# Kernel optimization log

Measured on AMD Instinct MI355X. Metric: run time of the kernel, lower is better.

## Reference

```python
import jax, jax.numpy as jnp
import numpy as np

DIM = 384
HEADS = 6
DIM_HEAD = 64
INNER = HEADS * DIM_HEAD  # 384


def setup_inputs() -> dict:
    key = jax.random.key(0)
    ks = jax.random.split(key, 6)
    s = 0.02
    return {
        "x_q": jax.random.normal(ks[0], (8, 4096, DIM), dtype=jnp.float32),
        "x_kv": jax.random.normal(ks[1], (8, 4096, DIM), dtype=jnp.float32),
        "Wq": jax.random.normal(ks[2], (DIM, INNER), dtype=jnp.float32) * s,
        "Wkv": jax.random.normal(ks[3], (DIM, 2 * INNER), dtype=jnp.float32) * s,
        "Wout": jax.random.normal(ks[4], (INNER, DIM), dtype=jnp.float32) * s,
        "bout": jax.random.normal(ks[5], (DIM,), dtype=jnp.float32) * s,
    }


def _split_heads(t, b, n):
    # [b, n, h*d] -> [b, h, n, d]
    return t.reshape(b, n, HEADS, DIM_HEAD).transpose(0, 2, 1, 3)


def reference(x_q, x_kv, Wq, Wkv, Wout, bout):
    b, nq, _ = x_q.shape
    nkv = x_kv.shape[1]
    q = x_q @ Wq                      # [b, nq, inner]
    kv_proj = x_kv @ Wkv              # [b, nkv, 2*inner]
    k, v = jnp.split(kv_proj, 2, axis=-1)
    q = _split_heads(q, b, nq)        # [b, h, nq, d]
    k = _split_heads(k, b, nkv)       # [b, h, nkv, d]
    v = _split_heads(v, b, nkv)       # [b, h, nkv, d]
    q = jax.nn.elu(q) + 1.0
    k = jax.nn.elu(k) + 1.0
    kv = jnp.einsum('bhnd,bhnm->bhdm', k, v)             # [b, h, d, d]
    z = 1.0 / (jnp.einsum('bhnd,bhd->bhn', q, k.sum(axis=2)) + 1e-6)
    out = jnp.einsum('bhnd,bhdm->bhnm', q, kv) * z[..., None]  # [b, h, nq, d]
    out = out.transpose(0, 2, 1, 3).reshape(b, nq, INNER)
    return out @ Wout + bout
```

## Files before the change

### kernel.cpp

```cpp
#include <hip/hip_runtime.h>
#include <math.h>

#define BATCH 8
#define SEQ 4096
#define DIMSZ 384
#define HEADS 6
#define DH 64
#define MTOT (BATCH * SEQ)
#define KD 384

typedef short short8 __attribute__((ext_vector_type(8)));
typedef float floatx4 __attribute__((ext_vector_type(4)));
typedef unsigned short ushort8v __attribute__((ext_vector_type(8)));
typedef unsigned int uint2v __attribute__((ext_vector_type(2)));
typedef unsigned int uint4v __attribute__((ext_vector_type(4)));

__device__ __forceinline__ float elu1(float x) { return x > 0.f ? x + 1.f : __expf(x); }

__device__ __forceinline__ unsigned short f2b(float f) {
    unsigned int u = __float_as_uint(f);
    u = (u + 0x7fffu + ((u >> 16) & 1u)) >> 16;
    return (unsigned short)u;
}
__device__ __forceinline__ unsigned int f2b2(float lo, float hi) {
    unsigned int r;
    asm("v_cvt_pk_bf16_f32 %0, %1, %2" : "=v"(r) : "v"(lo), "v"(hi));
    return r;
}

__device__ __forceinline__ void gl16(const void* g, void* l) {
    __builtin_amdgcn_global_load_lds((const __attribute__((address_space(1))) unsigned int*)g,
                                     (__attribute__((address_space(3))) unsigned int*)l, 16, 0, 0);
}

#define SB0() __builtin_amdgcn_sched_barrier(0)
#define BAR_SOFT()                     \
    do {                               \
        SB0();                         \
        __builtin_amdgcn_s_barrier();  \
        SB0();                         \
    } while (0)
#define BAR_STAGE()                                                 \
    do {                                                            \
        asm volatile("s_waitcnt vmcnt(0) lgkmcnt(0)" ::: "memory"); \
        __builtin_amdgcn_s_barrier();                               \
        SB0();                                                      \
    } while (0)

__global__ __launch_bounds__(256) void conv_wt3(const float* __restrict__ Wq,
                                                const float* __restrict__ Wkv,
                                                const float* __restrict__ Wout,
                                                unsigned short* __restrict__ WqT,
                                                unsigned short* __restrict__ WkvT,
                                                unsigned short* __restrict__ WoutT) {
    __shared__ float tile[32][33];
    int bx = blockIdx.x;
    const float* W;
    unsigned short* WT;
    int N;
    if (bx < 12) { W = Wq; WT = WqT; N = DIMSZ; }
    else if (bx < 36) { W = Wkv; WT = WkvT; N = 2 * DIMSZ; bx -= 12; }
    else { W = Wout; WT = WoutT; N = DIMSZ; bx -= 36; }
    const int n0 = bx * 32, k0 = blockIdx.y * 32;
    const int tx = threadIdx.x & 31, ty = threadIdx.x >> 5;
#pragma unroll
    for (int i = 0; i < 32; i += 8) tile[ty + i][tx] = W[(size_t)(k0 + ty + i) * N + n0 + tx];
    __syncthreads();
#pragma unroll
    for (int i = 0; i < 32; i += 8)
        WT[(size_t)(n0 + ty + i) * KD + k0 + tx] = f2b(tile[tx][ty + i]);
}

__global__ __launch_bounds__(256, 3) void gemm_kv(const float* __restrict__ A,
                                                  const unsigned short* __restrict__ WkvT,
                                                  float* __restrict__ pkv,
                                                  float* __restrict__ pks) {
    __shared__ __align__(16) unsigned short buf[24576];
    __shared__ float ksLDS[128];
    unsigned short* As = buf;
    unsigned short* Bs0 = buf + 8192;
    unsigned short* Bs1 = buf + 16384;
    const int tid = threadIdx.x;
    const int lane = tid & 63, wave = tid >> 6;
    const int l15 = lane & 15, qd = lane >> 4;
    const int fid = blockIdx.x;
    const int xcd = fid & 7;
    const int s = fid >> 3;
    const int h = s % HEADS;
    const int rtl = s / HEADS;
    const int row0 = (xcd * 32 + rtl) * 128;
    const int pidx = (xcd * HEADS + h) * 32 + rtl;
    const int wm = (wave & 1) * 64, wn = (wave >> 1) * 64;

    const float* Ab = A + (size_t)row0 * KD;
    const unsigned short* Bb = WkvT + (size_t)(h * DH) * KD;
    const int srow = tid >> 3;
    const int scol = (((tid & 7) ^ (srow & 7)) * 8);

    floatx4 zero = {0.f, 0.f, 0.f, 0.f};
    floatx4 acc[4][4];
#pragma unroll
    for (int i = 0; i < 4; ++i)
#pragma unroll
        for (int j = 0; j < 4; ++j) acc[i][j] = zero;

    const int sw = l15 & 7;
    float4 g0[4], g1[4];
#pragma unroll
    for (int i = 0; i < 4; ++i)
        gl16(Bb + (size_t)(i * 32 + srow + (i >= 2 ? 320 : 0)) * KD + scol,
             Bs0 + i * 2048 + wave * 512);
#pragma unroll
    for (int i = 0; i < 4; ++i) {
        const float* src = Ab + (size_t)(i * 32 + srow) * KD + scol;
        g0[i] = *(const float4*)src;
        g1[i] = *(const float4*)(src + 4);
    }
#pragma unroll
    for (int i = 0; i < 4; ++i) {
        uint4v u;
        u[0] = f2b2(g0[i].x, g0[i].y);
        u[1] = f2b2(g0[i].z, g0[i].w);
        u[2] = f2b2(g1[i].x, g1[i].y);
        u[3] = f2b2(g1[i].z, g1[i].w);
        *(uint4v*)&As[i * 2048 + tid * 8] = u;
    }
    BAR_STAGE();

#pragma unroll
    for (int t = 0; t < 6; ++t) {
        unsigned short* Bc = (t & 1) ? Bs1 : Bs0;
        if (t < 5) {
            unsigned short* Bn = (t & 1) ? Bs0 : Bs1;
            const int kn = t * 64 + 64;
#pragma unroll
            for (int i = 0; i < 4; ++i)
                gl16(Bb + (size_t)(i * 32 + srow + (i >= 2 ? 320 : 0)) * KD + kn + scol,
                     Bn + i * 2048 + wave * 512);
#pragma unroll
            for (int i = 0; i < 4; ++i) {
                const float* src = Ab + (size_t)(i * 32 + srow) * KD + kn + scol;
                g0[i] = *(const float4*)src;
                g1[i] = *(const float4*)(src + 4);
            }
            SB0();
        }
#pragma unroll
        for (int tt = 0; tt < 2; ++tt) {
            const int chnk = ((tt * 4 + qd) ^ sw) * 8;
            short8 af[4], bfr[4];
#pragma unroll
            for (int mi = 0; mi < 4; ++mi)
                af[mi] = *(const short8*)&As[(wm + mi * 16 + l15) * 64 + chnk];
#pragma unroll
            for (int ni = 0; ni < 4; ++ni)
                bfr[ni] = *(const short8*)&Bc[(wn + ni * 16 + l15) * 64 + chnk];
#pragma unroll
            for (int mi = 0; mi < 4; ++mi)
#pragma unroll
                for (int ni = 0; ni < 4; ++ni)
                    acc[mi][ni] = __builtin_amdgcn_mfma_f32_16x16x32_bf16(af[mi], bfr[ni],
                                                                          acc[mi][ni], 0, 0, 0);
        }
        if (t < 5) {
            BAR_SOFT();
#pragma unroll
            for (int i = 0; i < 4; ++i) {
                uint4v u;
                u[0] = f2b2(g0[i].x, g0[i].y);
                u[1] = f2b2(g0[i].z, g0[i].w);
                u[2] = f2b2(g1[i].x, g1[i].y);
                u[3] = f2b2(g1[i].z, g1[i].w);
                *(uint4v*)&As[i * 2048 + tid * 8] = u;
            }
            BAR_STAGE();
        }
    }

    __syncthreads();
    const bool kw = (wn == 0);
    float ksp[4] = {};
#pragma unroll
    for (int mi = 0; mi < 4; ++mi)
#pragma unroll
        for (int ni = 0; ni < 4; ++ni) {
            const int rb = wm + mi * 16 + qd * 4;
            const int cl = wn + ni * 16 + l15;
            float v0 = acc[mi][ni][0], v1 = acc[mi][ni][1];
            float v2 = acc[mi][ni][2], v3 = acc[mi][ni][3];
            if (kw) {
                v0 = elu1(v0); v1 = elu1(v1); v2 = elu1(v2); v3 = elu1(v3);
                ksp[ni] += (v0 + v1) + (v2 + v3);
            }
            uint2v o;
            o[0] = f2b2(v0, v1);
            o[1] = f2b2(v2, v3);
            *(uint2v*)&buf[cl * 136 + rb] = o;
        }
    if (kw) {
#pragma unroll
        for (int ni = 0; ni < 4; ++ni) {
            float v = ksp[ni];
            v += __shfl_xor(v, 16);
            v += __shfl_xor(v, 32);
            if (lane < 16) ksLDS[wave * 64 + ni * 16 + lane] = v;
        }
    }
    __syncthreads();
    floatx4 kva[4];
#pragma unroll
    for (int j = 0; j < 4; ++j) kva[j] = zero;
#pragma unroll
    for (int nk = 0; nk < 4; ++nk) {
        short8 afk = *(const short8*)&buf[(wave * 16 + l15) * 136 + nk * 32 + qd * 8];
#pragma unroll
        for (int nj = 0; nj < 4; ++nj) {
            short8 bfv = *(const short8*)&buf[(64 + nj * 16 + l15) * 136 + nk * 32 + qd * 8];
            kva[nj] = __builtin_amdgcn_mfma_f32_16x16x32_bf16(afk, bfv, kva[nj], 0, 0, 0);
        }
    }
    float* P = pkv + (size_t)pidx * 4096;
#pragma unroll
    for (int nj = 0; nj < 4; ++nj)
#pragma unroll
        for (int r = 0; r < 4; ++r)
            P[(wave * 16 + qd * 4 + r) * 64 + nj * 16 + l15] = kva[nj][r];
    if (tid < 64) pks[pidx * 64 + tid] = ksLDS[tid] + ksLDS[64 + tid];
}

__global__ __launch_bounds__(256) void kv_reduce(const float* __restrict__ pkv,
                                                 const float* __restrict__ pks,
                                                 unsigned short* __restrict__ kv_bf,
                                                 float* __restrict__ ksum_g) {
    const int bh = blockIdx.x >> 2, dc = blockIdx.x & 3;
    const int tid = threadIdx.x;
    unsigned short* kb = kv_bf + (size_t)bh * 4096;
    const int i0 = dc * 1024 + tid * 4;
    float4 sum = {0.f, 0.f, 0.f, 0.f};
#pragma unroll
    for (int c = 0; c < 32; ++c) {
        float4 p = *(const float4*)&pkv[(size_t)(bh * 32 + c) * 4096 + i0];
        sum.x += p.x; sum.y += p.y; sum.z += p.z; sum.w += p.w;
    }
    const int d = i0 >> 6, m = i0 & 63;
    kb[(m + 0) * 64 + d] = f2b(sum.x);
    kb[(m + 1) * 64 + d] = f2b(sum.y);
    kb[(m + 2) * 64 + d] = f2b(sum.z);
    kb[(m + 3) * 64 + d] = f2b(sum.w);
    if (dc == 0 && tid < 64) {
        float s = 0.f;
#pragma unroll
        for (int c = 0; c < 32; ++c) s += pks[(bh * 32 + c) * 64 + tid];
        ksum_g[bh * 64 + tid] = s;
    }
}

__global__ __launch_bounds__(256, 3) void gemm_q_attn(const float* __restrict__ A,
                                                      const unsigned short* __restrict__ WqT,
                                                      const unsigned short* __restrict__ kv_bf,
                                                      const float* __restrict__ ksum_g,
                                                      unsigned short* __restrict__ attn) {
    __shared__ __align__(16) unsigned short buf[24576];
    __shared__ float ksh[128];
    __shared__ float zsh[256];
    unsigned short* As = buf;
    unsigned short* Bs0 = buf + 8192;
    unsigned short* Bs1 = buf + 16384;
    const int tid = threadIdx.x;
    const int lane = tid & 63, wave = tid >> 6;
    const int l15 = lane & 15, qd = lane >> 4;
    const int fid = blockIdx.x;
    const int xcd = fid & 7;
    const int s = fid >> 3;
    const int ct = s % 3;
    const int rtl = s / 3;
    const int row0 = (xcd * 32 + rtl) * 128;
    const int col0 = ct * 128;
    const int bh0 = xcd * HEADS + ct * 2;
    const int wd = (wave & 1) * 64, wn2 = (wave >> 1) * 64;

    if (tid < 128) ksh[tid] = ksum_g[bh0 * 64 + tid];

    const float* Ab = A + (size_t)row0 * KD;
    const unsigned short* Bb = WqT + (size_t)col0 * KD;
    const int srow = tid >> 3;
    const int scol = (((tid & 7) ^ (srow & 7)) * 8);

    floatx4 zero = {0.f, 0.f, 0.f, 0.f};
    floatx4 acc[4][4];
#pragma unroll
    for (int i = 0; i < 4; ++i)
#pragma unroll
        for (int j = 0; j < 4; ++j) acc[i][j] = zero;

    const int sw = l15 & 7;
    float4 g0[4], g1[4];
#pragma unroll
    for (int i = 0; i < 4; ++i)
        gl16(Bb + (size_t)(i * 32 + srow) * KD + scol, Bs0 + i * 2048 + wave * 512);
#pragma unroll
    for (int i = 0; i < 4; ++i) {
        const float* src = Ab + (size_t)(i * 32 + srow) * KD + scol;
        g0[i] = *(const float4*)src;
        g1[i] = *(const float4*)(src + 4);
    }
#pragma unroll
    for (int i = 0; i < 4; ++i) {
        uint4v u;
        u[0] = f2b2(g0[i].x, g0[i].y);
        u[1] = f2b2(g0[i].z, g0[i].w);
        u[2] = f2b2(g1[i].x, g1[i].y);
        u[3] = f2b2(g1[i].z, g1[i].w);
        *(uint4v*)&As[i * 2048 + tid * 8] = u;
    }
    BAR_STAGE();

#pragma unroll
    for (int t = 0; t < 6; ++t) {
        unsigned short* Bc = (t & 1) ? Bs1 : Bs0;
        if (t < 5) {
            unsigned short* Bn = (t & 1) ? Bs0 : Bs1;
            const int kn = t * 64 + 64;
#pragma unroll
            for (int i = 0; i < 4; ++i)
                gl16(Bb + (size_t)(i * 32 + srow) * KD + kn + scol, Bn + i * 2048 + wave * 512);
#pragma unroll
            for (int i = 0; i < 4; ++i) {
                const float* src = Ab + (size_t)(i * 32 + srow) * KD + kn + scol;
                g0[i] = *(const float4*)src;
                g1[i] = *(const float4*)(src + 4);
            }
            SB0();
        }
#pragma unroll
        for (int tt = 0; tt < 2; ++tt) {
            const int chnk = ((tt * 4 + qd) ^ sw) * 8;
            short8 wf[4], xf[4];
#pragma unroll
            for (int di = 0; di < 4; ++di)
                wf[di] = *(const short8*)&Bc[(wd + di * 16 + l15) * 64 + chnk];
#pragma unroll
            for (int nj = 0; nj < 4; ++nj)
                xf[nj] = *(const short8*)&As[(wn2 + nj * 16 + l15) * 64 + chnk];
#pragma unroll
            for (int di = 0; di < 4; ++di)
#pragma unroll
                for (int nj = 0; nj < 4; ++nj)
                    acc[di][nj] = __builtin_amdgcn_mfma_f32_16x16x32_bf16(wf[di], xf[nj],
                                                                          acc[di][nj], 0, 0, 0);
        }
        if (t < 5) {
            BAR_SOFT();
#pragma unroll
            for (int i = 0; i < 4; ++i) {
                uint4v u;
                u[0] = f2b2(g0[i].x, g0[i].y);
                u[1] = f2b2(g0[i].z, g0[i].w);
                u[2] = f2b2(g1[i].x, g1[i].y);
                u[3] = f2b2(g1[i].z, g1[i].w);
                *(uint4v*)&As[i * 2048 + tid * 8] = u;
            }
            BAR_STAGE();
        }
    }

    float zp[4] = {};
#pragma unroll
    for (int di = 0; di < 4; ++di)
#pragma unroll
        for (int r = 0; r < 4; ++r) {
            const float ks = ksh[wd + di * 16 + qd * 4 + r];
#pragma unroll
            for (int nj = 0; nj < 4; ++nj) {
                const float q = elu1(acc[di][nj][r]);
                acc[di][nj][r] = q;
                zp[nj] += q * ks;
            }
        }
#pragma unroll
    for (int nj = 0; nj < 4; ++nj) {
        float v = zp[nj];
        v += __shfl_xor(v, 16);
        v += __shfl_xor(v, 32);
        zp[nj] = 1.f / (v + 1e-6f);
    }
    __syncthreads();
    if (lane < 16) {
#pragma unroll
        for (int nj = 0; nj < 4; ++nj) zsh[(wave & 1) * 128 + wn2 + nj * 16 + lane] = zp[nj];
    }
#pragma unroll
    for (int di = 0; di < 4; ++di)
#pragma unroll
        for (int nj = 0; nj < 4; ++nj) {
            const int rb = wd + di * 16 + qd * 4;
            const int cl = wn2 + nj * 16 + l15;
            uint2v o;
            o[0] = f2b2(acc[di][nj][0], acc[di][nj][1]);
            o[1] = f2b2(acc[di][nj][2], acc[di][nj][3]);
            *(uint2v*)&buf[cl * 136 + rb] = o;
        }
    __syncthreads();
    const int hh = wave & 1;
    const unsigned short* kvB = kv_bf + (size_t)(bh0 + hh) * 4096;
    floatx4 acc2[4][4];
#pragma unroll
    for (int i = 0; i < 4; ++i)
#pragma unroll
        for (int j = 0; j < 4; ++j) acc2[i][j] = zero;
#pragma unroll
    for (int t = 0; t < 2; ++t) {
        short8 bf2[4];
#pragma unroll
        for (int bj = 0; bj < 4; ++bj)
            bf2[bj] = *(const short8*)&kvB[(bj * 16 + l15) * 64 + t * 32 + qd * 8];
#pragma unroll
        for (int ai = 0; ai < 4; ++ai) {
            short8 af =
                *(const short8*)&buf[(wn2 + ai * 16 + l15) * 136 + hh * 64 + t * 32 + qd * 8];
#pragma unroll
            for (int bj = 0; bj < 4; ++bj)
                acc2[ai][bj] =
                    __builtin_amdgcn_mfma_f32_16x16x32_bf16(af, bf2[bj], acc2[ai][bj], 0, 0, 0);
        }
    }
#pragma unroll
    for (int ai = 0; ai < 4; ++ai)
#pragma unroll
        for (int bj = 0; bj < 4; ++bj) {
            const int colg = col0 + hh * 64 + bj * 16 + l15;
#pragma unroll
            for (int r = 0; r < 4; ++r) {
                const int nl = wn2 + ai * 16 + qd * 4 + r;
                const float v = acc2[ai][bj][r] * zsh[hh * 128 + nl];
                attn[(size_t)(row0 + nl) * KD + colg] = f2b(v);
            }
        }
}

__global__ __launch_bounds__(256, 3) void gemm_out(const unsigned short* __restrict__ A,
                                                   const unsigned short* __restrict__ BT,
                                                   float* __restrict__ C,
                                                   const float* __restrict__ bias) {
    __shared__ __align__(16) unsigned short buf[24576];
    unsigned short* As = buf;
    unsigned short* Bs0 = buf + 8192;
    unsigned short* Bs1 = buf + 16384;
    const int tid = threadIdx.x;
    const int lane = tid & 63, wave = tid >> 6;
    const int l15 = lane & 15, qd = lane >> 4;
    const int fid = blockIdx.x;
    const int xcd = fid & 7;
    const int s = fid >> 3;
    const int row0 = (xcd * 32 + s / 3) * 128;
    const int col0 = (s % 3) * 128;
    const int wm = (wave & 1) * 64, wn = (wave >> 1) * 64;

    const unsigned short* Ab = A + (size_t)row0 * KD;
    const unsigned short* Bb = BT + (size_t)col0 * KD;
    const int srow = tid >> 3;
    const int scol = (((tid & 7) ^ (srow & 7)) * 8);

    floatx4 zero = {0.f, 0.f, 0.f, 0.f};
    floatx4 acc[4][4];
#pragma unroll
    for (int i = 0; i < 4; ++i)
#pragma unroll
        for (int j = 0; j < 4; ++j) acc[i][j] = zero;

    const int sw = l15 & 7;
    ushort8v ga[4];
#pragma unroll
    for (int i = 0; i < 4; ++i)
        gl16(Bb + (size_t)(i * 32 + srow) * KD + scol, Bs0 + i * 2048 + wave * 512);
#pragma unroll
    for (int i = 0; i < 4; ++i)
        ga[i] = *(const ushort8v*)(Ab + (size_t)(i * 32 + srow) * KD + scol);
#pragma unroll
    for (int i = 0; i < 4; ++i) *(ushort8v*)&As[i * 2048 + tid * 8] = ga[i];
    BAR_STAGE();

#pragma unroll
    for (int t = 0; t < 6; ++t) {
        unsigned short* Bc = (t & 1) ? Bs1 : Bs0;
        if (t < 5) {
            unsigned short* Bn = (t & 1) ? Bs0 : Bs1;
            const int kn = t * 64 + 64;
#pragma unroll
            for (int i = 0; i < 4; ++i)
                gl16(Bb + (size_t)(i * 32 + srow) * KD + kn + scol, Bn + i * 2048 + wave * 512);
#pragma unroll
            for (int i = 0; i < 4; ++i)
                ga[i] = *(const ushort8v*)(Ab + (size_t)(i * 32 + srow) * KD + kn + scol);
            SB0();
        }
#pragma unroll
        for (int tt = 0; tt < 2; ++tt) {
            const int chnk = ((tt * 4 + qd) ^ sw) * 8;
            short8 af[4], bfr[4];
#pragma unroll
            for (int mi = 0; mi < 4; ++mi)
                af[mi] = *(const short8*)&As[(wm + mi * 16 + l15) * 64 + chnk];
#pragma unroll
            for (int ni = 0; ni < 4; ++ni)
                bfr[ni] = *(const short8*)&Bc[(wn + ni * 16 + l15) * 64 + chnk];
#pragma unroll
            for (int mi = 0; mi < 4; ++mi)
#pragma unroll
                for (int ni = 0; ni < 4; ++ni)
                    acc[mi][ni] = __builtin_amdgcn_mfma_f32_16x16x32_bf16(af[mi], bfr[ni],
                                                                          acc[mi][ni], 0, 0, 0);
        }
        if (t < 5) {
            BAR_SOFT();
#pragma unroll
            for (int i = 0; i < 4; ++i) *(ushort8v*)&As[i * 2048 + tid * 8] = ga[i];
            BAR_STAGE();
        }
    }
#pragma unroll
    for (int mi = 0; mi < 4; ++mi)
#pragma unroll
        for (int ni = 0; ni < 4; ++ni) {
            const int rbase = row0 + wm + mi * 16 + qd * 4;
            const int col = col0 + wn + ni * 16 + l15;
            const float bsv = bias[col];
#pragma unroll
            for (int r = 0; r < 4; ++r)
                __builtin_nontemporal_store(acc[mi][ni][r] + bsv,
                                            &C[(size_t)(rbase + r) * DIMSZ + col]);
        }
}

extern "C" void kernel_launch(void* const* d_in, const int* in_sizes, int n_in,
                              void* d_out, int out_size, void* d_ws, size_t ws_size,
                              hipStream_t stream) {
    const float* x_q = (const float*)d_in[0];
    const float* x_kv = (const float*)d_in[1];
    const float* Wq = (const float*)d_in[2];
    const float* Wkv = (const float*)d_in[3];
    const float* Wout = (const float*)d_in[4];
    const float* bout = (const float*)d_in[5];
    float* out = (float*)d_out;

    char* ws = (char*)d_ws;
    float* pkv = (float*)(ws + 0);
    unsigned short* attn_bf = (unsigned short*)(ws + 0);
    unsigned short* WqT = (unsigned short*)(ws + 25165824);
    unsigned short* WkvT = (unsigned short*)(ws + 25460736);
    unsigned short* WoutT = (unsigned short*)(ws + 26050560);
    float* ksum = (float*)(ws + 26345472);
    float* pks = (float*)(ws + 26357760);
    unsigned short* kv_bf = (unsigned short*)(ws + 26750976);

    dim3 blk(256);
    conv_wt3<<<dim3(48, 12), blk, 0, stream>>>(Wq, Wkv, Wout, WqT, WkvT, WoutT);
    gemm_kv<<<dim3(1536), blk, 0, stream>>>(x_kv, WkvT, pkv, pks);
    kv_reduce<<<dim3(192), blk, 0, stream>>>(pkv, pks, kv_bf, ksum);
    gemm_q_attn<<<dim3(768), blk, 0, stream>>>(x_q, WqT, kv_bf, ksum, attn_bf);
    gemm_out<<<dim3(768), blk, 0, stream>>>(attn_bf, WoutT, out, bout);
}
```

Before: 216.2 us.

## Double-buffer A tiles and stage B through registers, dropping one barrier per step

```diff
diff --git a/kernel.cpp b/kernel.cpp
--- a/kernel.cpp
+++ b/kernel.cpp
@@ -28,23 +28,12 @@
     return r;
 }
 
-__device__ __forceinline__ void gl16(const void* g, void* l) {
-    __builtin_amdgcn_global_load_lds((const __attribute__((address_space(1))) unsigned int*)g,
-                                     (__attribute__((address_space(3))) unsigned int*)l, 16, 0, 0);
-}
-
 #define SB0() __builtin_amdgcn_sched_barrier(0)
-#define BAR_SOFT()                     \
-    do {                               \
-        SB0();                         \
-        __builtin_amdgcn_s_barrier();  \
-        SB0();                         \
-    } while (0)
-#define BAR_STAGE()                                                 \
-    do {                                                            \
-        asm volatile("s_waitcnt vmcnt(0) lgkmcnt(0)" ::: "memory"); \
-        __builtin_amdgcn_s_barrier();                               \
-        SB0();                                                      \
+#define BAR_LGKM()                                        \
+    do {                                                  \
+        asm volatile("s_waitcnt lgkmcnt(0)" ::: "memory");\
+        __builtin_amdgcn_s_barrier();                     \
+        SB0();                                            \
     } while (0)
 
 __global__ __launch_bounds__(256) void conv_wt3(const float* __restrict__ Wq,
@@ -71,15 +60,16 @@
         WT[(size_t)(n0 + ty + i) * KD + k0 + tx] = f2b(tile[tx][ty + i]);
 }
 
-__global__ __launch_bounds__(256, 3) void gemm_kv(const float* __restrict__ A,
+__global__ __launch_bounds__(256, 2) void gemm_kv(const float* __restrict__ A,
                                                   const unsigned short* __restrict__ WkvT,
                                                   float* __restrict__ pkv,
                                                   float* __restrict__ pks) {
-    __shared__ __align__(16) unsigned short buf[24576];
+    __shared__ __align__(16) unsigned short buf[32768];
     __shared__ float ksLDS[128];
-    unsigned short* As = buf;
-    unsigned short* Bs0 = buf + 8192;
-    unsigned short* Bs1 = buf + 16384;
+    unsigned short* As0 = buf;
+    unsigned short* As1 = buf + 8192;
+    unsigned short* Bs0 = buf + 16384;
+    unsigned short* Bs1 = buf + 24576;
     const int tid = threadIdx.x;
     const int lane = tid & 63, wave = tid >> 6;
     const int l15 = lane & 15, qd = lane >> 4;
@@ -106,15 +96,13 @@
 
     const int sw = l15 & 7;
     float4 g0[4], g1[4];
-#pragma unroll
-    for (int i = 0; i < 4; ++i)
-        gl16(Bb + (size_t)(i * 32 + srow + (i >= 2 ? 320 : 0)) * KD + scol,
-             Bs0 + i * 2048 + wave * 512);
+    ushort8v gb[4];
 #pragma unroll
     for (int i = 0; i < 4; ++i) {
         const float* src = Ab + (size_t)(i * 32 + srow) * KD + scol;
         g0[i] = *(const float4*)src;
         g1[i] = *(const float4*)(src + 4);
+        gb[i] = *(const ushort8v*)(Bb + (size_t)(i * 32 + srow + (i >= 2 ? 320 : 0)) * KD + scol);
     }
 #pragma unroll
     for (int i = 0; i < 4; ++i) {
@@ -123,25 +111,27 @@
         u[1] = f2b2(g0[i].z, g0[i].w);
         u[2] = f2b2(g1[i].x, g1[i].y);
         u[3] = f2b2(g1[i].z, g1[i].w);
-        *(uint4v*)&As[i * 2048 + tid * 8] = u;
-    }
-    BAR_STAGE();
+        *(uint4v*)&As0[i * 2048 + tid * 8] = u;
+        *(ushort8v*)&Bs0[i * 2048 + tid * 8] = gb[i];
+    }
+    BAR_LGKM();
 
 #pragma unroll
     for (int t = 0; t < 6; ++t) {
+        unsigned short* Ac = (t & 1) ? As1 : As0;
         unsigned short* Bc = (t & 1) ? Bs1 : Bs0;
+        unsigned short* An = (t & 1) ? As0 : As1;
+        unsigned short* Bn = (t & 1) ? Bs0 : Bs1;
         if (t < 5) {
-            unsigned short* Bn = (t & 1) ? Bs0 : Bs1;
-            const int kn = t * 64 + 64;
-#pragma unroll
-            for (int i = 0; i < 4; ++i)
-                gl16(Bb + (size_t)(i * 32 + srow + (i >= 2 ? 320 : 0)) * KD + kn + scol,
-                     Bn + i * 2048 + wave * 512);
+            const int kn = (t + 1) * 64;
 #pragma unroll
             for (int i = 0; i < 4; ++i) {
                 const float* src = Ab + (size_t)(i * 32 + srow) * KD + kn + scol;
                 g0[i] = *(const float4*)src;
                 g1[i] = *(const float4*)(src + 4);
+                gb[i] = *(const ushort8v*)(Bb +
+                                           (size_t)(i * 32 + srow + (i >= 2 ? 320 : 0)) * KD +
+                                           kn + scol);
             }
             SB0();
         }
@@ -151,7 +141,7 @@
             short8 af[4], bfr[4];
 #pragma unroll
             for (int mi = 0; mi < 4; ++mi)
-                af[mi] = *(const short8*)&As[(wm + mi * 16 + l15) * 64 + chnk];
+                af[mi] = *(const short8*)&Ac[(wm + mi * 16 + l15) * 64 + chnk];
 #pragma unroll
             for (int ni = 0; ni < 4; ++ni)
                 bfr[ni] = *(const short8*)&Bc[(wn + ni * 16 + l15) * 64 + chnk];
@@ -163,7 +153,6 @@
                                                                           acc[mi][ni], 0, 0, 0);
         }
         if (t < 5) {
-            BAR_SOFT();
 #pragma unroll
             for (int i = 0; i < 4; ++i) {
                 uint4v u;
@@ -171,9 +160,10 @@
                 u[1] = f2b2(g0[i].z, g0[i].w);
                 u[2] = f2b2(g1[i].x, g1[i].y);
                 u[3] = f2b2(g1[i].z, g1[i].w);
-                *(uint4v*)&As[i * 2048 + tid * 8] = u;
-            }
-            BAR_STAGE();
+                *(uint4v*)&An[i * 2048 + tid * 8] = u;
+                *(ushort8v*)&Bn[i * 2048 + tid * 8] = gb[i];
+            }
+            BAR_LGKM();
         }
     }
 
@@ -255,17 +245,18 @@
     }
 }
 
-__global__ __launch_bounds__(256, 3) void gemm_q_attn(const float* __restrict__ A,
+__global__ __launch_bounds__(256, 2) void gemm_q_attn(const float* __restrict__ A,
                                                       const unsigned short* __restrict__ WqT,
                                                       const unsigned short* __restrict__ kv_bf,
                                                       const float* __restrict__ ksum_g,
                                                       unsigned short* __restrict__ attn) {
-    __shared__ __align__(16) unsigned short buf[24576];
+    __shared__ __align__(16) unsigned short buf[32768];
     __shared__ float ksh[128];
     __shared__ float zsh[256];
-    unsigned short* As = buf;
-    unsigned short* Bs0 = buf + 8192;
-    unsigned short* Bs1 = buf + 16384;
+    unsigned short* As0 = buf;
+    unsigned short* As1 = buf + 8192;
+    unsigned short* Bs0 = buf + 16384;
+    unsigned short* Bs1 = buf + 24576;
     const int tid = threadIdx.x;
     const int lane = tid & 63, wave = tid >> 6;
     const int l15 = lane & 15, qd = lane >> 4;
@@ -295,14 +286,13 @@
 
     const int sw = l15 & 7;
     float4 g0[4], g1[4];
-#pragma unroll
-    for (int i = 0; i < 4; ++i)
-        gl16(Bb + (size_t)(i * 32 + srow) * KD + scol, Bs0 + i * 2048 + wave * 512);
+    ushort8v gb[4];
 #pragma unroll
     for (int i = 0; i < 4; ++i) {
         const float* src = Ab + (size_t)(i * 32 + srow) * KD + scol;
         g0[i] = *(const float4*)src;
         g1[i] = *(const float4*)(src + 4);
+        gb[i] = *(const ushort8v*)(Bb + (size_t)(i * 32 + srow) * KD + scol);
     }
 #pragma unroll
     for (int i = 0; i < 4; ++i) {
@@ -311,24 +301,25 @@
         u[1] = f2b2(g0[i].z, g0[i].w);
         u[2] = f2b2(g1[i].x, g1[i].y);
         u[3] = f2b2(g1[i].z, g1[i].w);
-        *(uint4v*)&As[i * 2048 + tid * 8] = u;
-    }
-    BAR_STAGE();
+        *(uint4v*)&As0[i * 2048 + tid * 8] = u;
+        *(ushort8v*)&Bs0[i * 2048 + tid * 8] = gb[i];
+    }
+    BAR_LGKM();
 
 #pragma unroll
     for (int t = 0; t < 6; ++t) {
+        unsigned short* Ac = (t & 1) ? As1 : As0;
         unsigned short* Bc = (t & 1) ? Bs1 : Bs0;
+        unsigned short* An = (t & 1) ? As0 : As1;
+        unsigned short* Bn = (t & 1) ? Bs0 : Bs1;
         if (t < 5) {
-            unsigned short* Bn = (t & 1) ? Bs0 : Bs1;
-            const int kn = t * 64 + 64;
-#pragma unroll
-            for (int i = 0; i < 4; ++i)
-                gl16(Bb + (size_t)(i * 32 + srow) * KD + kn + scol, Bn + i * 2048 + wave * 512);
+            const int kn = (t + 1) * 64;
 #pragma unroll
             for (int i = 0; i < 4; ++i) {
                 const float* src = Ab + (size_t)(i * 32 + srow) * KD + kn + scol;
                 g0[i] = *(const float4*)src;
                 g1[i] = *(const float4*)(src + 4);
+                gb[i] = *(const ushort8v*)(Bb + (size_t)(i * 32 + srow) * KD + kn + scol);
             }
             SB0();
         }
@@ -341,7 +332,7 @@
                 wf[di] = *(const short8*)&Bc[(wd + di * 16 + l15) * 64 + chnk];
 #pragma unroll
             for (int nj = 0; nj < 4; ++nj)
-                xf[nj] = *(const short8*)&As[(wn2 + nj * 16 + l15) * 64 + chnk];
+                xf[nj] = *(const short8*)&Ac[(wn2 + nj * 16 + l15) * 64 + chnk];
 #pragma unroll
             for (int di = 0; di < 4; ++di)
 #pragma unroll
@@ -350,7 +341,6 @@
                                                                           acc[di][nj], 0, 0, 0);
         }
         if (t < 5) {
-            BAR_SOFT();
 #pragma unroll
             for (int i = 0; i < 4; ++i) {
                 uint4v u;
@@ -358,9 +348,10 @@
                 u[1] = f2b2(g0[i].z, g0[i].w);
                 u[2] = f2b2(g1[i].x, g1[i].y);
                 u[3] = f2b2(g1[i].z, g1[i].w);
-                *(uint4v*)&As[i * 2048 + tid * 8] = u;
-            }
-            BAR_STAGE();
+                *(uint4v*)&An[i * 2048 + tid * 8] = u;
+                *(ushort8v*)&Bn[i * 2048 + tid * 8] = gb[i];
+            }
+            BAR_LGKM();
         }
     }
 
@@ -438,14 +429,15 @@
         }
 }
 
-__global__ __launch_bounds__(256, 3) void gemm_out(const unsigned short* __restrict__ A,
+__global__ __launch_bounds__(256, 2) void gemm_out(const unsigned short* __restrict__ A,
                                                    const unsigned short* __restrict__ BT,
                                                    float* __restrict__ C,
                                                    const float* __restrict__ bias) {
-    __shared__ __align__(16) unsigned short buf[24576];
-    unsigned short* As = buf;
-    unsigned short* Bs0 = buf + 8192;
-    unsigned short* Bs1 = buf + 16384;
+    __shared__ __align__(16) unsigned short buf[32768];
+    unsigned short* As0 = buf;
+    unsigned short* As1 = buf + 8192;
+    unsigned short* Bs0 = buf + 16384;
+    unsigned short* Bs1 = buf + 24576;
     const int tid = threadIdx.x;
     const int lane = tid & 63, wave = tid >> 6;
     const int l15 = lane & 15, qd = lane >> 4;
@@ -469,29 +461,32 @@
         for (int j = 0; j < 4; ++j) acc[i][j] = zero;
 
     const int sw = l15 & 7;
-    ushort8v ga[4];
-#pragma unroll
-    for (int i = 0; i < 4; ++i)
-        gl16(Bb + (size_t)(i * 32 + srow) * KD + scol, Bs0 + i * 2048 + wave * 512);
-#pragma unroll
-    for (int i = 0; i < 4; ++i)
+    ushort8v ga[4], gb[4];
+#pragma unroll
+    for (int i = 0; i < 4; ++i) {
         ga[i] = *(const ushort8v*)(Ab + (size_t)(i * 32 + srow) * KD + scol);
-#pragma unroll
-    for (int i = 0; i < 4; ++i) *(ushort8v*)&As[i * 2048 + tid * 8] = ga[i];
-    BAR_STAGE();
+        gb[i] = *(const ushort8v*)(Bb + (size_t)(i * 32 + srow) * KD + scol);
+    }
+#pragma unroll
+    for (int i = 0; i < 4; ++i) {
+        *(ushort8v*)&As0[i * 2048 + tid * 8] = ga[i];
+        *(ushort8v*)&Bs0[i * 2048 + tid * 8] = gb[i];
+    }
+    BAR_LGKM();
 
 #pragma unroll
     for (int t = 0; t < 6; ++t) {
+        unsigned short* Ac = (t & 1) ? As1 : As0;
         unsigned short* Bc = (t & 1) ? Bs1 : Bs0;
+        unsigned short* An = (t & 1) ? As0 : As1;
+        unsigned short* Bn = (t & 1) ? Bs0 : Bs1;
         if (t < 5) {
-            unsigned short* Bn = (t & 1) ? Bs0 : Bs1;
-            const int kn = t * 64 + 64;
-#pragma unroll
-            for (int i = 0; i < 4; ++i)
-                gl16(Bb + (size_t)(i * 32 + srow) * KD + kn + scol, Bn + i * 2048 + wave * 512);
-#pragma unroll
-            for (int i = 0; i < 4; ++i)
+            const int kn = (t + 1) * 64;
+#pragma unroll
+            for (int i = 0; i < 4; ++i) {
                 ga[i] = *(const ushort8v*)(Ab + (size_t)(i * 32 + srow) * KD + kn + scol);
+                gb[i] = *(const ushort8v*)(Bb + (size_t)(i * 32 + srow) * KD + kn + scol);
+            }
             SB0();
         }
 #pragma unroll
@@ -500,7 +495,7 @@
             short8 af[4], bfr[4];
 #pragma unroll
             for (int mi = 0; mi < 4; ++mi)
-                af[mi] = *(const short8*)&As[(wm + mi * 16 + l15) * 64 + chnk];
+                af[mi] = *(const short8*)&Ac[(wm + mi * 16 + l15) * 64 + chnk];
 #pragma unroll
             for (int ni = 0; ni < 4; ++ni)
                 bfr[ni] = *(const short8*)&Bc[(wn + ni * 16 + l15) * 64 + chnk];
@@ -512,10 +507,12 @@
                                                                           acc[mi][ni], 0, 0, 0);
         }
         if (t < 5) {
-            BAR_SOFT();
-#pragma unroll
-            for (int i = 0; i < 4; ++i) *(ushort8v*)&As[i * 2048 + tid * 8] = ga[i];
-            BAR_STAGE();
+#pragma unroll
+            for (int i = 0; i < 4; ++i) {
+                *(ushort8v*)&An[i * 2048 + tid * 8] = ga[i];
+                *(ushort8v*)&Bn[i * 2048 + tid * 8] = gb[i];
+            }
+            BAR_LGKM();
         }
     }
 #pragma unroll
```

Measured after the change: 223.8 us. 1.04x slower.
